# Performance work log

Hardware: AMD Instinct MI355X
Metric: run time of the kernel (lower is better)

## Reference

```python
import jax, jax.numpy as jnp
import numpy as np

B, C, T, H, W = 4, 256, 64, 32, 32
K = 64  # kernel_size spans the whole sequence


def setup_inputs() -> dict:
    key = jax.random.key(0)
    kx, kw = jax.random.split(key)
    x = jax.random.normal(kx, (B, C, T, H, W), dtype=jnp.float32)
    # nn.Parameter(torch.randn(channels, 1, kernel_size) * 0.01)
    weight = jax.random.normal(kw, (C, 1, K), dtype=jnp.float32) * 0.01
    return {"x": x, "weight": weight}


def reference(x, weight):
    b, c, t, h, w = x.shape
    k = weight.shape[-1]
    pad = k - 1
    # torch .view: raw row-major reinterpretation of (B,C,T,H,W) as (B*H*W, C, T)
    x_ = x.reshape(b * h * w, c, t)
    # depthwise (groups=C) cross-correlation, symmetric padding like F.conv1d(padding=pad)
    y = jax.lax.conv_general_dilated(
        x_, weight,
        window_strides=(1,),
        padding=[(pad, pad)],
        feature_group_count=c,
        dimension_numbers=("NCH", "OIH", "NCH"),
    )  # (B*H*W, C, T + pad)
    y = y[:, :, -t:]  # causal slice: keep last T positions
    # .view(B,H,W,C,T).permute(0,3,4,1,2) -> (B,C,T,H,W)
    y = y.reshape(b, h, w, c, t).transpose(0, 3, 4, 1, 2)
    return y
```

## Files before the change

kernel.cpp:

```cpp
#include <hip/hip_runtime.h>


constexpr int Cc = 256;
constexpr int Tt = 64;
constexpr int Kk = 64;
constexpr int CT = Cc * Tt;
constexpr int CHUNK_STRIDE = 1024 + 16;
constexpr int LDS_BYTES = 16 * CHUNK_STRIDE;

__global__ __launch_bounds__(64, 2)
void DepthwiseTemporalConv_24962349924982_kernel(const float* __restrict__ x,
                                                 const float* __restrict__ w,
                                                 float* __restrict__ out) {
    __shared__ __align__(16) char lds[LDS_BYTES];
    const int lane = threadIdx.x & 63;

    const int n_tile = blockIdx.x & 63;
    const int c      = blockIdx.x >> 6;
    const int n0 = n_tile * 64;
    const int n  = n0 + lane;

    #pragma unroll
    for (int i = 0; i < 16; ++i) {
        const float* gsrc = x + (size_t)(n0 + 4 * i + (lane >> 4)) * CT
                              + (size_t)c * Tt + (lane & 15) * 4;
        __builtin_amdgcn_global_load_lds(
            (const __attribute__((address_space(1))) void*)gsrc,
            (__attribute__((address_space(3))) void*)(lds + i * CHUNK_STRIDE),
            16, 0, 0);
    }

    float wr[Kk];
    {
        const float4* wp = (const float4*)(w + (size_t)c * Kk);
        #pragma unroll
        for (int m = 0; m < 16; ++m) {
            const float4 v = wp[m];
            wr[4*m+0] = v.x; wr[4*m+1] = v.y; wr[4*m+2] = v.z; wr[4*m+3] = v.w;
        }
    }

    asm volatile("s_waitcnt vmcnt(0)" ::: "memory");
    __builtin_amdgcn_sched_barrier(0);

    float xr[Tt];
    {
        const char* base = lds + (lane >> 2) * CHUNK_STRIDE + (lane & 3) * 256;
        #pragma unroll
        for (int m = 0; m < 16; ++m) {
            const float4 v = *(const float4*)(base + m * 16);
            xr[4*m+0] = v.x; xr[4*m+1] = v.y; xr[4*m+2] = v.z; xr[4*m+3] = v.w;
        }
    }

    float* __restrict__ obase = out + (size_t)(n >> 10) * (Cc * Tt * 1024)
                                    + (size_t)c * (Tt * 1024) + (n & 1023);
    #pragma unroll
    for (int t = 0; t < Tt; ++t) {
        const int len = Tt - t;
        float a0 = 0.f, a1 = 0.f;
        #pragma unroll
        for (int k = 0; k + 1 < len; k += 2) {
            a0 = fmaf(xr[t + k],     wr[k],     a0);
            a1 = fmaf(xr[t + k + 1], wr[k + 1], a1);
        }
        if (len & 1) a0 = fmaf(xr[Tt - 1], wr[len - 1], a0);
        obase[(size_t)t * 1024] = a0 + a1;
    }
}

extern "C" void kernel_launch(void* const* d_in, const int* in_sizes, int n_in,
                              void* d_out, int out_size, void* d_ws, size_t ws_size,
                              hipStream_t stream) {
    const float* x = (const float*)d_in[0];
    const float* w = (const float*)d_in[1];
    float* out = (float*)d_out;
    DepthwiseTemporalConv_24962349924982_kernel<<<dim3(16384), dim3(64), 0, stream>>>(x, w, out);
}
```

Measured before the change: 147.9 us.

## Load input rows directly into registers and remap blocks channel-fastest

Drops the LDS staging path, so each thread issues sixteen 16-byte global loads of its own 256-byte row straight into registers through inline asm. Blocks grow to 128 threads, launch bounds go to 5 waves per EU, and the block index now varies channel fastest. The channel is made wave-uniform with readfirstlane. The aim is to cut the LDS round trip and raise occupancy, but each lane now reads a strided row, which may coalesce worse than the earlier cooperative chunked loads.

```diff
diff --git a/kernel.cpp b/kernel.cpp
--- a/kernel.cpp
+++ b/kernel.cpp
@@ -5,34 +5,32 @@
 constexpr int Tt = 64;
 constexpr int Kk = 64;
 constexpr int CT = Cc * Tt;
-constexpr int CHUNK_STRIDE = 1024 + 16;
-constexpr int LDS_BYTES = 16 * CHUNK_STRIDE;
 
-__global__ __launch_bounds__(64, 2)
+typedef float f32x4 __attribute__((ext_vector_type(4)));
+
+__global__ __launch_bounds__(128, 5)
 void DepthwiseTemporalConv_24962349924982_kernel(const float* __restrict__ x,
                                                  const float* __restrict__ w,
                                                  float* __restrict__ out) {
-    __shared__ __align__(16) char lds[LDS_BYTES];
-    const int lane = threadIdx.x & 63;
+    const int tid = threadIdx.x;
+    const int bid = blockIdx.x;
+    const int c      = bid & 255;
+    const int n_tile = bid >> 8;
+    const int n  = n_tile * 128 + tid;
+    const int cu = __builtin_amdgcn_readfirstlane(c);
 
-    const int n_tile = blockIdx.x & 63;
-    const int c      = blockIdx.x >> 6;
-    const int n0 = n_tile * 64;
-    const int n  = n0 + lane;
-
+    const float* rowp = x + (size_t)n * CT + (size_t)cu * Tt;
+    f32x4 q[16];
     #pragma unroll
-    for (int i = 0; i < 16; ++i) {
-        const float* gsrc = x + (size_t)(n0 + 4 * i + (lane >> 4)) * CT
-                              + (size_t)c * Tt + (lane & 15) * 4;
-        __builtin_amdgcn_global_load_lds(
-            (const __attribute__((address_space(1))) void*)gsrc,
-            (__attribute__((address_space(3))) void*)(lds + i * CHUNK_STRIDE),
-            16, 0, 0);
+    for (int m = 0; m < 16; ++m) {
+        asm volatile("global_load_dwordx4 %0, %1, off offset:%2"
+                     : "=v"(q[m])
+                     : "v"(rowp), "i"(16 * m));
     }
 
     float wr[Kk];
     {
-        const float4* wp = (const float4*)(w + (size_t)c * Kk);
+        const float4* wp = (const float4*)(w + (size_t)cu * Kk);
         #pragma unroll
         for (int m = 0; m < 16; ++m) {
             const float4 v = wp[m];
@@ -44,17 +42,14 @@
     __builtin_amdgcn_sched_barrier(0);
 
     float xr[Tt];
-    {
-        const char* base = lds + (lane >> 2) * CHUNK_STRIDE + (lane & 3) * 256;
-        #pragma unroll
-        for (int m = 0; m < 16; ++m) {
-            const float4 v = *(const float4*)(base + m * 16);
-            xr[4*m+0] = v.x; xr[4*m+1] = v.y; xr[4*m+2] = v.z; xr[4*m+3] = v.w;
-        }
+    #pragma unroll
+    for (int m = 0; m < 16; ++m) {
+        xr[4*m+0] = q[m][0]; xr[4*m+1] = q[m][1];
+        xr[4*m+2] = q[m][2]; xr[4*m+3] = q[m][3];
     }
 
     float* __restrict__ obase = out + (size_t)(n >> 10) * (Cc * Tt * 1024)
-                                    + (size_t)c * (Tt * 1024) + (n & 1023);
+                                    + (size_t)cu * (Tt * 1024) + (n & 1023);
     #pragma unroll
     for (int t = 0; t < Tt; ++t) {
         const int len = Tt - t;
@@ -75,5 +70,5 @@
     const float* x = (const float*)d_in[0];
     const float* w = (const float*)d_in[1];
     float* out = (float*)d_out;
-    DepthwiseTemporalConv_24962349924982_kernel<<<dim3(16384), dim3(64), 0, stream>>>(x, w, out);
+    DepthwiseTemporalConv_24962349924982_kernel<<<dim3(8192), dim3(128), 0, stream>>>(x, w, out);
 }
```

Measured after the change: 144.8 us. 2.1% less time.
